# Performance work log

Hardware: AMD Instinct MI355X
Metric: run time of the kernel (lower is better)

## Reference

```python
import jax, jax.numpy as jnp
import numpy as np

B, N, D, DFC, EMB, L = 16, 1024, 128, 128, 64, 4
NHOPS = (1, 2, 3, 4)  # tatic='cont': nhop(i) = i + 1
EDGE_P = 0.03


def _make_adj(k):
    u = jax.random.uniform(k, (B, N, N))
    a = u < EDGE_P
    a = a | jnp.transpose(a, (0, 2, 1))          # undirected
    a = a | jnp.eye(N, dtype=bool)[None]         # self loops
    return a.astype(jnp.float32)


def setup_inputs() -> dict:
    key = jax.random.key(0)
    ks = jax.random.split(key, 16)
    s = 0.05
    x = jax.random.normal(ks[0], (B, N, 2 * EMB), jnp.float32)
    adj1 = _make_adj(ks[1])
    adj2 = _make_adj(ks[2])
    valid = jnp.ones((B, N), jnp.float32)
    embede_w = jax.random.normal(ks[3], (D, 2 * EMB)) * s
    gW = jax.random.normal(ks[4], (L, D, D)) * s
    gb = jnp.zeros((L, D), jnp.float32)
    gA = jax.random.normal(ks[5], (L, D, D)) * s
    gate_w = jax.random.normal(ks[6], (L, 1, 2 * D)) * s
    gate_b = jnp.zeros((L, 1), jnp.float32)
    fc0_w = jax.random.normal(ks[7], (DFC, D)) * s
    fc0_b = jnp.zeros((DFC,), jnp.float32)
    fc1_w = jax.random.normal(ks[8], (DFC, DFC)) * s
    fc1_b = jnp.zeros((DFC,), jnp.float32)
    fc2_w = jax.random.normal(ks[9], (DFC, DFC)) * s
    fc2_b = jnp.zeros((DFC,), jnp.float32)
    fc3_w = jax.random.normal(ks[10], (1, DFC)) * s
    fc3_b = jnp.zeros((1,), jnp.float32)
    return dict(x=x, adj1=adj1, adj2=adj2, valid=valid, embede_w=embede_w,
                gW=gW, gb=gb, gA=gA, gate_w=gate_w, gate_b=gate_b,
                fc0_w=fc0_w, fc0_b=fc0_b, fc1_w=fc1_w, fc1_b=fc1_b,
                fc2_w=fc2_w, fc2_b=fc2_b, fc3_w=fc3_w, fc3_b=fc3_b)


def _glema(x, adj, W, b, A, gw, gbias, nhop):
    h = x @ W.T + b                                        # [B,N,D]
    e = jnp.einsum('bjl,bkl->bjk', jnp.einsum('bjd,de->bje', h, A), h)
    e = e + jnp.transpose(e, (0, 2, 1))                    # undirected
    att = jnp.where(adj > 0, e, jnp.float32(0.0))
    att = jax.nn.softmax(att, axis=1) * adj                # softmax over dim 1, then adj mask
    az = jax.nn.relu(jnp.einsum('bij,bjd->bid', att, h))
    coeff = jax.nn.sigmoid(jnp.concatenate([h, az], -1) @ gw.T + gbias)  # [B,N,1]
    z = h
    for _ in range(nhop):
        az = jax.nn.relu(jnp.einsum('bij,bjd->bid', att, z))
        z = coeff * h + (1.0 - coeff) * az
    return z


def reference(x, adj1, adj2, valid, embede_w, gW, gb, gA, gate_w, gate_b,
              fc0_w, fc0_b, fc1_w, fc1_b, fc2_w, fc2_b, fc3_w, fc3_b):
    h = x @ embede_w.T                                     # embede (no bias)
    for k in range(L):                                     # branch='both': c_hs2 - c_hs1
        h1 = _glema(h, adj1, gW[k], gb[k], gA[k], gate_w[k], gate_b[k], NHOPS[k])
        h2 = _glema(h, adj2, gW[k], gb[k], gA[k], gate_w[k], gate_b[k], NHOPS[k])
        h = h2 - h1                                        # dropout p used in eval mode -> identity
    h = h * valid[..., None]
    pooled = h.sum(1) / valid.sum(1, keepdims=True)        # [B,D]
    y = jax.nn.relu(pooled @ fc0_w.T + fc0_b)
    y = jax.nn.relu(y @ fc1_w.T + fc1_b)
    y = jax.nn.relu(y @ fc2_w.T + fc2_b)
    y = jax.nn.sigmoid(y @ fc3_w.T + fc3_b)
    return y.reshape(-1)                                   # [B]
```

## Files before the change

kernel.cpp:

```cpp
#include <hip/hip_runtime.h>

typedef _Float16 half_t;
typedef _Float16 half8 __attribute__((ext_vector_type(8)));
typedef _Float16 half4v __attribute__((ext_vector_type(4)));
typedef float floatx4 __attribute__((ext_vector_type(4)));

#define MFMA(a,b,c) __builtin_amdgcn_mfma_f32_16x16x32_f16(a,b,c,0,0,0)

#define NB 16
#define NLEN 1024
#define DD 128
#define BN (NB*NLEN)
#define BND ((size_t)NB*NLEN*DD)
#define BNN ((size_t)NB*NLEN*NLEN)
#define ELLS 128
#define EMP 1044

static __device__ inline float f16lo(unsigned pk) {
    unsigned short us = (unsigned short)(pk & 0xffffu);
    half_t h; __builtin_memcpy(&h, &us, 2); return (float)h;
}
static __device__ inline half_t f16h(unsigned pk) {
    unsigned short us = (unsigned short)(pk & 0xffffu);
    half_t h; __builtin_memcpy(&h, &us, 2); return h;
}

__global__ __launch_bounds__(256)
void k_prep(const float* __restrict__ x, const float* __restrict__ Ew, half_t* __restrict__ h16,
            const float* __restrict__ gW, const float* __restrict__ gA,
            half_t* __restrict__ Wf, half_t* __restrict__ STf) {
    int tid = threadIdx.x;
    if (blockIdx.x >= 2048) {
        int i = (blockIdx.x - 2048) * 256 + tid;
        Wf[i] = (half_t)gW[i];
        int base = i & ~16383;
        int lrem = i & 16383;
        int d = lrem >> 7, e = lrem & 127;
        STf[base + (e << 7) + d] = (half_t)(gA[i] + gA[base + (e << 7) + d]);
        return;
    }
    __shared__ float rows[8][DD];
    int g = blockIdx.x * 8;
    {
        int nl = tid >> 5, c4 = (tid & 31) * 4;
        *(float4*)&rows[nl][c4] = *(const float4*)&x[(size_t)(g + nl) * DD + c4];
    }
    __syncthreads();
    int t = tid & 127, half = tid >> 7;
    const float* wr = Ew + (size_t)t * DD;
    float acc[4] = {0.f, 0.f, 0.f, 0.f};
    for (int k = 0; k < DD; k++) {
        float w = wr[k];
#pragma unroll
        for (int m = 0; m < 4; m++) acc[m] += rows[half + 2 * m][k] * w;
    }
#pragma unroll
    for (int m = 0; m < 4; m++) h16[(size_t)(g + half + 2 * m) * DD + t] = (half_t)acc[m];
}

__global__ __launch_bounds__(256)
void k_ell(const float* __restrict__ adj1, const float* __restrict__ adj2,
           unsigned* __restrict__ ell, unsigned* __restrict__ cntA) {
    int t = threadIdx.x, w = t >> 6, l = t & 63;
    int R = blockIdx.x * 4 + w;
    int br = R >> 14, nb = R & 16383;
    const float* arow = (br ? adj2 : adj1) + (size_t)nb * 1024;
    unsigned* erow = ell + (size_t)R * ELLS;
    unsigned long long lmask = (l == 0) ? 0ull : (~0ull >> (64 - l));
    int base = 0;
#pragma unroll
    for (int ch = 0; ch < 4; ch++) {
        float4 v = *(const float4*)&arow[ch * 256 + l * 4];
        float vals[4] = {v.x, v.y, v.z, v.w};
#pragma unroll
        for (int comp = 0; comp < 4; comp++) {
            bool pred = vals[comp] > 0.f;
            unsigned long long b = __ballot(pred);
            if (pred) {
                int idx = base + __popcll(b & lmask);
                if (idx < ELLS) erow[idx] = ((unsigned)(ch * 256 + l * 4 + comp)) << 16;
            }
            base += __popcll(b);
        }
    }
    if (base > ELLS) base = ELLS;
    if (l == 0) cntA[R] = (unsigned)base;
    for (int s = base + l; s < ELLS; s += 64) erow[s] = 0u;
}

__global__ __launch_bounds__(256)
void k_proj(const half_t* __restrict__ pa, const half_t* __restrict__ pb,
            const half_t* __restrict__ Wf, const float* __restrict__ bias,
            const half_t* __restrict__ STf,
            half_t* __restrict__ hbr16, half_t* __restrict__ hbrF, half_t* __restrict__ hSF) {
    __shared__ half_t htile[32 * 136];
    __shared__ half_t hbtile[32 * 136];
    int g = blockIdx.x * 32;
    int t = threadIdx.x;
    int w = t >> 6, l = t & 63, q = l >> 4, l15 = l & 15;
#pragma unroll
    for (int v = 0; v < 2; v++) {
        int idx = v * 256 + t; int r = idx >> 4, c8 = (idx & 15) * 8;
        half8 va = *(const half8*)&pa[((size_t)(g + r) << 7) + c8];
        if (pb) {
            half8 vb = *(const half8*)&pb[((size_t)(g + r) << 7) + c8];
            va = va - vb;
        }
        *(half8*)&htile[r * 136 + c8] = va;
    }
    __syncthreads();
    int rowh = (w & 1) * 16;
    int c0 = (w >> 1) * 4;
    half8 a1[4];
#pragma unroll
    for (int kc = 0; kc < 4; kc++) a1[kc] = *(const half8*)&htile[(rowh + l15) * 136 + kc * 32 + q * 8];
    floatx4 acc[4];
#pragma unroll
    for (int cc = 0; cc < 4; cc++) {
        int col = (c0 + cc) * 16 + l15;
        floatx4 a = {0.f, 0.f, 0.f, 0.f};
#pragma unroll
        for (int kc = 0; kc < 4; kc++) {
            half8 bf = *(const half8*)&Wf[((size_t)col << 7) + kc * 32 + q * 8];
            a = MFMA(a1[kc], bf, a);
        }
        float bv = bias[col];
        a.x += bv; a.y += bv; a.z += bv; a.w += bv;
        acc[cc] = a;
    }
#pragma unroll
    for (int cc = 0; cc < 4; cc++) {
        int col = (c0 + cc) * 16 + l15;
#pragma unroll
        for (int r = 0; r < 4; r++)
            hbtile[(rowh + q * 4 + r) * 136 + col] = (half_t)acc[cc][r];
    }
    __syncthreads();
    half8 a2[4];
#pragma unroll
    for (int kc = 0; kc < 4; kc++) a2[kc] = *(const half8*)&hbtile[(rowh + l15) * 136 + kc * 32 + q * 8];
#pragma unroll
    for (int cc = 0; cc < 4; cc++) {
        int col = (c0 + cc) * 16 + l15;
        floatx4 a = {0.f, 0.f, 0.f, 0.f};
#pragma unroll
        for (int kc = 0; kc < 4; kc++) {
            half8 bf = *(const half8*)&STf[((size_t)col << 7) + kc * 32 + q * 8];
            a = MFMA(a2[kc], bf, a);
        }
        acc[cc] = a;
    }
    __syncthreads();
#pragma unroll
    for (int cc = 0; cc < 4; cc++) {
        int col = (c0 + cc) * 16 + l15;
#pragma unroll
        for (int r = 0; r < 4; r++) htile[(rowh + q * 4 + r) * 136 + col] = (half_t)acc[cc][r];
    }
    __syncthreads();
#pragma unroll
    for (int v = 0; v < 2; v++) {
        int idx = v * 256 + t; int r = idx >> 4, c8 = (idx & 15) * 8;
        *(half8*)&hbr16[((size_t)(g + r) << 7) + c8] = *(const half8*)&hbtile[r * 136 + c8];
    }
#pragma unroll
    for (int v = 0; v < 2; v++) {
        int fi = v * 256 + t;
        int g2 = fi >> 8, kc = (fi >> 6) & 3, li = fi & 63;
        int src = (g2 * 16 + (li & 15)) * 136 + kc * 32 + (li >> 4) * 8;
        size_t dst = (((size_t)(blockIdx.x * 2 + g2) * 4 + kc) << 10) + li * 8;
        *(half8*)&hbrF[dst] = *(const half8*)&hbtile[src];
        *(half8*)&hSF[dst]  = *(const half8*)&htile[src];
    }
}

__global__ __launch_bounds__(256)
void k_E(const half_t* __restrict__ hSF, const half_t* __restrict__ hbrF,
         const half_t* __restrict__ hbr16,
         unsigned* __restrict__ ell, const unsigned* __restrict__ cntA,
         float* __restrict__ rsr, half_t* __restrict__ hbrs) {
    int b = blockIdx.y, s = blockIdx.x;
    int t = threadIdx.x, w = t >> 6, l = t & 63, q = l >> 4, l15 = l & 15;
    __shared__ half_t emS[16 * EMP];
    __shared__ float rsS[2][16];
    size_t Gb = (size_t)b * 64;
    half8 A[4];
#pragma unroll
    for (int kc = 0; kc < 4; kc++)
        A[kc] = *(const half8*)&hSF[(((Gb + s) * 4 + kc) << 10) + l * 8];
#pragma unroll 4
    for (int cg = 0; cg < 16; cg++) {
        int c0 = w * 256 + cg * 16;
        floatx4 a = {0.f, 0.f, 0.f, 0.f};
#pragma unroll
        for (int kc = 0; kc < 4; kc++) {
            half8 bf = *(const half8*)&hbrF[(((Gb + w * 16 + cg) * 4 + kc) << 10) + l * 8];
            a = MFMA(A[kc], bf, a);
        }
#pragma unroll
        for (int r = 0; r < 4; r++)
            emS[(q * 4 + r) * EMP + c0 + l15] = (half_t)a[r];
    }
    __syncthreads();
    const float CN = 0.000335462627903f;
#pragma unroll
    for (int rr = 0; rr < 4; rr++) {
        int rl = w * 4 + rr;
        int rowg = b * 1024 + s * 16 + rl;
#pragma unroll
        for (int br = 0; br < 2; br++) {
            size_t R = ((size_t)br << 14) + rowg;
            int cn = (int)cntA[R];
            float rs = 0.f;
            for (int base = 0; base < cn; base += 64) {
                int si = base + l;
                float v = 0.f;
                if (si < cn) {
                    unsigned pk = ell[R * ELLS + si];
                    int col = (int)(pk >> 16);
                    float em = (float)emS[rl * EMP + col];
                    v = __expf(em - 8.f);
                    half_t hv = (half_t)v;
                    unsigned short us; __builtin_memcpy(&us, &hv, 2);
                    ((unsigned short*)ell)[(R * ELLS + si) * 2] = us;
                }
                rs += v;
            }
            rs += __shfl_xor(rs, 1); rs += __shfl_xor(rs, 2);
            rs += __shfl_xor(rs, 4); rs += __shfl_xor(rs, 8);
            rs += __shfl_xor(rs, 16); rs += __shfl_xor(rs, 32);
            if (l == 0) {
                float rv = 1.f / (rs + (1024.f - (float)cn) * CN);
                rsr[R] = rv;
                rsS[br][rl] = rv;
            }
        }
    }
    __syncthreads();
    const half_t* hrow = hbr16 + ((size_t)b << 17) + ((size_t)(s * 16) << 7);
#pragma unroll
    for (int v = 0; v < 2; v++) {
        int idx = v * 256 + t;
        int row = idx >> 5, br2 = (idx >> 4) & 1, ch = idx & 15;
        half8 hv = *(const half8*)&hrow[(size_t)row * 128 + ch * 8];
        float sc = rsS[br2][row];
        half8 o;
#pragma unroll
        for (int d = 0; d < 8; d++) o[d] = (half_t)(sc * (float)hv[d]);
        *(half8*)&hbrs[(size_t)br2 * BND + ((size_t)(b * 1024 + s * 16 + row) << 7) + ch * 8] = o;
    }
}

__global__ __launch_bounds__(256)
void k_az(const unsigned* __restrict__ ell, const unsigned* __restrict__ cntA,
          const float* __restrict__ rsr,
          const half_t* __restrict__ zin, const half_t* __restrict__ hbr16,
          const float* __restrict__ gw, const float* __restrict__ gb_,
          float* __restrict__ cfb, half_t* __restrict__ outp, int mode) {
    int t = threadIdx.x, w = t >> 6, l = t & 63;
    int g = l >> 4, l15 = l & 15;
    int R = blockIdx.x * 16 + w * 4 + g;
    int br = R >> 14, nb = R & 16383;
    const unsigned* ep = ell + (size_t)R * ELLS;
    int cn = (int)cntA[R];
    const half_t* zb = zin + (size_t)br * BND + (((size_t)(nb & ~1023)) << 7) + l15 * 8;
    half8 acc8 = {};
    for (int s = 0; s < cn; s += 4) {
        uint4 p4 = *(const uint4*)(ep + s);
        unsigned pk[4] = {p4.x, p4.y, p4.z, p4.w};
#pragma unroll
        for (int i = 0; i < 4; i++) {
            half8 zz = *(const half8*)(zb + (((size_t)(pk[i] >> 16)) << 7));
            half_t hv = f16h(pk[i]);
            half8 vv = {hv, hv, hv, hv, hv, hv, hv, hv};
            acc8 += zz * vv;
        }
    }
    float acc[8];
#pragma unroll
    for (int d = 0; d < 8; d++) acc[d] = fmaxf((float)acc8[d], 0.f);
    half8 hv8 = *(const half8*)&hbr16[((size_t)nb << 7) + l15 * 8];
    float hv[8];
#pragma unroll
    for (int d = 0; d < 8; d++) hv[d] = (float)hv8[d];
    float cf;
    if (mode >= 3) {
        const float* g1 = gw + l15 * 8;
        const float* g2 = gw + 128 + l15 * 8;
        float dp = 0.f;
#pragma unroll
        for (int d = 0; d < 8; d++) dp += hv[d] * g1[d] + acc[d] * g2[d];
        dp += __shfl_xor(dp, 1); dp += __shfl_xor(dp, 2);
        dp += __shfl_xor(dp, 4); dp += __shfl_xor(dp, 8);
        cf = 1.f / (1.f + __expf(-(dp + gb_[0])));
        if (l15 == 0) cfb[R] = cf;
    } else {
        cf = cfb[R];
    }
    float sc = (mode == 1 || mode == 3) ? rsr[R] : 1.f;
    half8 o;
#pragma unroll
    for (int d = 0; d < 8; d++)
        o[d] = (half_t)(sc * (cf * hv[d] + (1.f - cf) * acc[d]));
    *(half8*)&outp[(size_t)R * DD + l15 * 8] = o;
}

__global__ __launch_bounds__(256)
void k_pool(const half_t* __restrict__ z2, const half_t* __restrict__ z1,
            const float* __restrict__ valid, float* __restrict__ part) {
    int b = blockIdx.y, s = blockIdx.x;
    int t = threadIdx.x, d = t & 127, hf = t >> 7;
    __shared__ float red[128];
    float acc = 0.f;
    int nbase = s * 128 + hf * 64;
    for (int n = nbase; n < nbase + 64; n++) {
        size_t gi = ((size_t)(b * 1024 + n) << 7) + d;
        acc += ((float)z2[gi] - (float)z1[gi]) * valid[b * 1024 + n];
    }
    if (hf) red[d] = acc;
    __syncthreads();
    if (!hf) part[(b * 8 + s) * 128 + d] = acc + red[d];
}

__global__ __launch_bounds__(128)
void k_mlp(const float* __restrict__ part, const float* __restrict__ valid,
           const float* __restrict__ w0, const float* __restrict__ b0,
           const float* __restrict__ w1, const float* __restrict__ b1,
           const float* __restrict__ w2, const float* __restrict__ b2,
           const float* __restrict__ w3, const float* __restrict__ b3,
           float* __restrict__ out) {
    int b = blockIdx.x, t = threadIdx.x;
    __shared__ float y0[DD], y1[DD];
    __shared__ float sred[2];
    float vs = 0.f;
    for (int n = t; n < NLEN; n += 128) vs += valid[b * NLEN + n];
    for (int off = 32; off; off >>= 1) vs += __shfl_down(vs, off);
    if ((t & 63) == 0) sred[t >> 6] = vs;
    __syncthreads();
    float vsum = sred[0] + sred[1];
    float acc = 0.f;
#pragma unroll
    for (int s = 0; s < 8; s++) acc += part[(b * 8 + s) * 128 + t];
    y0[t] = acc / vsum;
    __syncthreads();
    float a = b0[t];
    for (int k = 0; k < DD; k++) a += y0[k] * w0[t * DD + k];
    y1[t] = fmaxf(a, 0.f);
    __syncthreads();
    a = b1[t];
    for (int k = 0; k < DD; k++) a += y1[k] * w1[t * DD + k];
    y0[t] = fmaxf(a, 0.f);
    __syncthreads();
    a = b2[t];
    for (int k = 0; k < DD; k++) a += y0[k] * w2[t * DD + k];
    y1[t] = fmaxf(a, 0.f);
    __syncthreads();
    float p = y1[t] * w3[t];
    for (int off = 32; off; off >>= 1) p += __shfl_down(p, off);
    if ((t & 63) == 0) sred[t >> 6] = p;
    __syncthreads();
    if (t == 0) out[b] = 1.f / (1.f + __expf(-(sred[0] + sred[1] + b3[0])));
}

extern "C" void kernel_launch(void* const* d_in, const int* in_sizes, int n_in,
                              void* d_out, int out_size, void* d_ws, size_t ws_size,
                              hipStream_t stream) {
    (void)in_sizes; (void)n_in; (void)out_size; (void)ws_size;
    const float* x     = (const float*)d_in[0];
    const float* adj1  = (const float*)d_in[1];
    const float* adj2  = (const float*)d_in[2];
    const float* valid = (const float*)d_in[3];
    const float* Ew    = (const float*)d_in[4];
    const float* gW    = (const float*)d_in[5];
    const float* gb    = (const float*)d_in[6];
    const float* gA    = (const float*)d_in[7];
    const float* gatew = (const float*)d_in[8];
    const float* gateb = (const float*)d_in[9];
    const float* w0 = (const float*)d_in[10]; const float* b0 = (const float*)d_in[11];
    const float* w1 = (const float*)d_in[12]; const float* b1 = (const float*)d_in[13];
    const float* w2 = (const float*)d_in[14]; const float* b2 = (const float*)d_in[15];
    const float* w3 = (const float*)d_in[16]; const float* b3 = (const float*)d_in[17];
    float* out = (float*)d_out;

    char* p = (char*)d_ws;
    float* rsr  = (float*)p; p += 2 * BN * 4;
    float* cfb  = (float*)p; p += 2 * BN * 4;
    float* partb = (float*)p; p += (size_t)NB * 8 * 128 * 4;
    half_t* h16   = (half_t*)p; p += BND * 2;
    half_t* hbr16 = (half_t*)p; p += BND * 2;
    half_t* hbrF  = (half_t*)p; p += BND * 2;
    half_t* hSF   = (half_t*)p; p += BND * 2;
    half_t* hbrs  = (half_t*)p; p += 2 * BND * 2;
    half_t* zf    = (half_t*)p; p += 2 * BND * 2;
    half_t* zsA   = (half_t*)p; p += 2 * BND * 2;
    half_t* zsB   = (half_t*)p; p += 2 * BND * 2;
    unsigned* ell = (unsigned*)p; p += (size_t)2 * BN * ELLS * 4;
    unsigned* cntA = (unsigned*)p; p += (size_t)2 * BN * 4;
    half_t* Wf16 = (half_t*)p; p += (size_t)4 * 128 * 128 * 2;
    half_t* ST16 = (half_t*)p; p += (size_t)4 * 128 * 128 * 2;

    k_prep<<<2304, 256, 0, stream>>>(x, Ew, h16, gW, gA, Wf16, ST16);
    k_ell<<<8192, 256, 0, stream>>>(adj1, adj2, ell, cntA);

    for (int k = 0; k < 4; k++) {
        int nhop = k + 1;
        const half_t* pa = k ? (zf + BND) : h16;
        const half_t* pb = k ? zf : nullptr;
        k_proj<<<512, 256, 0, stream>>>(pa, pb, Wf16 + (size_t)k * 16384, gb + k * 128,
                                        ST16 + (size_t)k * 16384, hbr16, hbrF, hSF);
        k_E<<<dim3(64, NB), 256, 0, stream>>>(hSF, hbrF, hbr16, ell, cntA, rsr, hbrs);
        half_t* tgate = (nhop == 1) ? zf : zsA;
        k_az<<<2048, 256, 0, stream>>>(ell, cntA, rsr, hbrs, hbr16,
                                       gatew + k * 256, gateb + k, cfb, tgate,
                                       (nhop == 1) ? 4 : 3);
        half_t* src = tgate;
        for (int hop = 2; hop <= nhop; hop++) {
            half_t* dst = (hop == nhop) ? zf : ((hop & 1) ? zsA : zsB);
            k_az<<<2048, 256, 0, stream>>>(ell, cntA, rsr, src, hbr16,
                                           gatew + k * 256, gateb + k, cfb, dst,
                                           (hop == nhop) ? 2 : 1);
            src = dst;
        }
    }
    k_pool<<<dim3(8, NB), 256, 0, stream>>>(zf + BND, zf, valid, partb);
    k_mlp<<<16, 128, 0, stream>>>(partb, valid, w0, b0, w1, b1, w2, b2, w3, b3, out);
}
```

Measured before the change: 702.5 us.

## Fuse ELL build into prep kernel, stage ELL rows in LDS, prefetch indices

Merges the adjacency-to-ELL conversion and the embedding/weight prep into one launch, so one kernel launch and its tail disappear and the two kinds of work can overlap. ELL rows are now built in shared memory and written out with coalesced uint2 stores, replacing scattered global stores plus a separate zero-fill loop. The k_az neighbour loop software-prefetches the next packed index quad, so the ELL buffer is padded by 16 bytes to keep the over-read in bounds. Adjacency reads of about 128MB dominate the prep, so the gain is likely limited to launch and store overhead.

Measured after the change: 697.4 us. No clear change (-0.7%).

```diff
diff --git a/kernel.cpp b/kernel.cpp
--- a/kernel.cpp
+++ b/kernel.cpp
@@ -16,22 +16,56 @@
 #define ELLS 128
 #define EMP 1044
 
-static __device__ inline float f16lo(unsigned pk) {
-    unsigned short us = (unsigned short)(pk & 0xffffu);
-    half_t h; __builtin_memcpy(&h, &us, 2); return (float)h;
-}
 static __device__ inline half_t f16h(unsigned pk) {
     unsigned short us = (unsigned short)(pk & 0xffffu);
     half_t h; __builtin_memcpy(&h, &us, 2); return h;
 }
 
 __global__ __launch_bounds__(256)
-void k_prep(const float* __restrict__ x, const float* __restrict__ Ew, half_t* __restrict__ h16,
-            const float* __restrict__ gW, const float* __restrict__ gA,
-            half_t* __restrict__ Wf, half_t* __restrict__ STf) {
+void k_pre(const float* __restrict__ adj1, const float* __restrict__ adj2,
+           unsigned* __restrict__ ell, unsigned* __restrict__ cntA,
+           const float* __restrict__ x, const float* __restrict__ Ew, half_t* __restrict__ h16,
+           const float* __restrict__ gW, const float* __restrict__ gA,
+           half_t* __restrict__ Wf, half_t* __restrict__ STf) {
     int tid = threadIdx.x;
-    if (blockIdx.x >= 2048) {
-        int i = (blockIdx.x - 2048) * 256 + tid;
+    int bid = blockIdx.x;
+    if (bid < 8192) {
+        __shared__ unsigned ebuf[4][ELLS];
+        int w = tid >> 6, l = tid & 63;
+        int R = bid * 4 + w;
+        int br = R >> 14, nb = R & 16383;
+        const float* arow = (br ? adj2 : adj1) + (size_t)nb * 1024;
+        unsigned* myb = ebuf[w];
+        myb[l] = 0u; myb[l + 64] = 0u;
+        float4 v0 = *(const float4*)&arow[l * 4];
+        float4 v1 = *(const float4*)&arow[256 + l * 4];
+        float4 v2 = *(const float4*)&arow[512 + l * 4];
+        float4 v3 = *(const float4*)&arow[768 + l * 4];
+        unsigned long long lmask = (l == 0) ? 0ull : (~0ull >> (64 - l));
+        int base = 0;
+        float vals[16] = {v0.x, v0.y, v0.z, v0.w, v1.x, v1.y, v1.z, v1.w,
+                          v2.x, v2.y, v2.z, v2.w, v3.x, v3.y, v3.z, v3.w};
+#pragma unroll
+        for (int ch = 0; ch < 4; ch++) {
+#pragma unroll
+            for (int comp = 0; comp < 4; comp++) {
+                bool pred = vals[ch * 4 + comp] > 0.f;
+                unsigned long long b = __ballot(pred);
+                if (pred) {
+                    int idx = base + __popcll(b & lmask);
+                    if (idx < ELLS) myb[idx] = ((unsigned)(ch * 256 + l * 4 + comp)) << 16;
+                }
+                base += __popcll(b);
+            }
+        }
+        if (base > ELLS) base = ELLS;
+        if (l == 0) cntA[R] = (unsigned)base;
+        uint2 o = {myb[l * 2], myb[l * 2 + 1]};
+        *(uint2*)&ell[(size_t)R * ELLS + l * 2] = o;
+        return;
+    }
+    if (bid >= 10240) {
+        int i = (bid - 10240) * 256 + tid;
         Wf[i] = (half_t)gW[i];
         int base = i & ~16383;
         int lrem = i & 16383;
@@ -40,7 +74,7 @@
         return;
     }
     __shared__ float rows[8][DD];
-    int g = blockIdx.x * 8;
+    int g = (bid - 8192) * 8;
     {
         int nl = tid >> 5, c4 = (tid & 31) * 4;
         *(float4*)&rows[nl][c4] = *(const float4*)&x[(size_t)(g + nl) * DD + c4];
@@ -56,36 +90,6 @@
     }
 #pragma unroll
     for (int m = 0; m < 4; m++) h16[(size_t)(g + half + 2 * m) * DD + t] = (half_t)acc[m];
-}
-
-__global__ __launch_bounds__(256)
-void k_ell(const float* __restrict__ adj1, const float* __restrict__ adj2,
-           unsigned* __restrict__ ell, unsigned* __restrict__ cntA) {
-    int t = threadIdx.x, w = t >> 6, l = t & 63;
-    int R = blockIdx.x * 4 + w;
-    int br = R >> 14, nb = R & 16383;
-    const float* arow = (br ? adj2 : adj1) + (size_t)nb * 1024;
-    unsigned* erow = ell + (size_t)R * ELLS;
-    unsigned long long lmask = (l == 0) ? 0ull : (~0ull >> (64 - l));
-    int base = 0;
-#pragma unroll
-    for (int ch = 0; ch < 4; ch++) {
-        float4 v = *(const float4*)&arow[ch * 256 + l * 4];
-        float vals[4] = {v.x, v.y, v.z, v.w};
-#pragma unroll
-        for (int comp = 0; comp < 4; comp++) {
-            bool pred = vals[comp] > 0.f;
-            unsigned long long b = __ballot(pred);
-            if (pred) {
-                int idx = base + __popcll(b & lmask);
-                if (idx < ELLS) erow[idx] = ((unsigned)(ch * 256 + l * 4 + comp)) << 16;
-            }
-            base += __popcll(b);
-        }
-    }
-    if (base > ELLS) base = ELLS;
-    if (l == 0) cntA[R] = (unsigned)base;
-    for (int s = base + l; s < ELLS; s += 64) erow[s] = 0u;
 }
 
 __global__ __launch_bounds__(256)
@@ -265,9 +269,11 @@
     int cn = (int)cntA[R];
     const half_t* zb = zin + (size_t)br * BND + (((size_t)(nb & ~1023)) << 7) + l15 * 8;
     half8 acc8 = {};
+    uint4 p4 = *(const uint4*)ep;
     for (int s = 0; s < cn; s += 4) {
-        uint4 p4 = *(const uint4*)(ep + s);
-        unsigned pk[4] = {p4.x, p4.y, p4.z, p4.w};
+        uint4 cur = p4;
+        p4 = *(const uint4*)(ep + s + 4);
+        unsigned pk[4] = {cur.x, cur.y, cur.z, cur.w};
 #pragma unroll
         for (int i = 0; i < 4; i++) {
             half8 zz = *(const half8*)(zb + (((size_t)(pk[i] >> 16)) << 7));
@@ -394,13 +400,12 @@
     half_t* zf    = (half_t*)p; p += 2 * BND * 2;
     half_t* zsA   = (half_t*)p; p += 2 * BND * 2;
     half_t* zsB   = (half_t*)p; p += 2 * BND * 2;
-    unsigned* ell = (unsigned*)p; p += (size_t)2 * BN * ELLS * 4;
+    unsigned* ell = (unsigned*)p; p += (size_t)2 * BN * ELLS * 4 + 16;
     unsigned* cntA = (unsigned*)p; p += (size_t)2 * BN * 4;
     half_t* Wf16 = (half_t*)p; p += (size_t)4 * 128 * 128 * 2;
     half_t* ST16 = (half_t*)p; p += (size_t)4 * 128 * 128 * 2;
 
-    k_prep<<<2304, 256, 0, stream>>>(x, Ew, h16, gW, gA, Wf16, ST16);
-    k_ell<<<8192, 256, 0, stream>>>(adj1, adj2, ell, cntA);
+    k_pre<<<10496, 256, 0, stream>>>(adj1, adj2, ell, cntA, x, Ew, h16, gW, gA, Wf16, ST16);
 
     for (int k = 0; k < 4; k++) {
         int nhop = k + 1;
```
